# Kernel tuning notes

Measured on AMD Instinct MI355X. Metric: run time of the kernel, lower is better.

## Reference

```python
import jax, jax.numpy as jnp
import numpy as np

E, K, D, H, C = 32768, 32, 128, 4, 10
DH = D // H

def setup_inputs() -> dict:
    key = jax.random.key(0)
    ks = jax.random.split(key, 9)
    s = 1.0 / np.sqrt(D)
    return {
        "edge_feats": jax.random.normal(ks[0], (E, D), jnp.float32),
        "Wq": jax.random.normal(ks[1], (D, D), jnp.float32) * s,
        "Wk": jax.random.normal(ks[2], (D, D), jnp.float32) * s,
        "Wv": jax.random.normal(ks[3], (D, D), jnp.float32) * s,
        "Wo": jax.random.normal(ks[4], (D, D), jnp.float32) * s,
        "W1": jax.random.normal(ks[5], (D, D), jnp.float32) * s,
        "b1": jnp.zeros((D,), jnp.float32),
        "W2": jax.random.normal(ks[6], (D, C), jnp.float32) * s,
        "b2": jnp.zeros((C,), jnp.float32),
        "edge_adj": jax.random.randint(ks[7], (E, K), 0, E, jnp.int32),
    }

def reference(edge_feats, Wq, Wk, Wv, Wo, W1, b1, W2, b2, edge_adj):
    # Edge attention: each edge attends over its K adjacent edges.
    q = (edge_feats @ Wq).reshape(E, H, DH)                 # [E,H,dh]
    k_all = edge_feats @ Wk                                  # [E,D]
    v_all = edge_feats @ Wv                                  # [E,D]
    kn = k_all[edge_adj].reshape(E, K, H, DH)                # gather [E,K,H,dh]
    vn = v_all[edge_adj].reshape(E, K, H, DH)                # gather [E,K,H,dh]
    scores = jnp.einsum("ehd,ekhd->ehk", q, kn) / np.sqrt(DH)
    attn = jax.nn.softmax(scores, axis=-1)                   # [E,H,K]
    ctx = jnp.einsum("ehk,ekhd->ehd", attn, vn).reshape(E, D)
    edge_out = ctx @ Wo                                       # [E,D]
    # classifier: Linear -> GELU -> Linear
    h = jax.nn.gelu(edge_out @ W1 + b1)
    logits = h @ W2 + b2                                      # [E,C]
    return logits
```

## Files before the change

### kernel.cpp

```cpp
#include <hip/hip_runtime.h>
#include <hip/hip_bf16.h>

constexpr int E_EDGES = 32768;
constexpr int DIM = 128;

using bf16x8 = __attribute__((ext_vector_type(8))) short;
using f32x4  = __attribute__((ext_vector_type(4))) float;
using f32x2  = __attribute__((ext_vector_type(2))) float;
typedef unsigned int uint4v __attribute__((ext_vector_type(4)));
typedef unsigned int uint2v __attribute__((ext_vector_type(2)));

__device__ inline float bflo(unsigned u) { return __uint_as_float(u << 16); }
__device__ inline float bfhi(unsigned u) { return __uint_as_float(u & 0xffff0000u); }
__device__ inline f32x2 bf2f2(unsigned u) {
    f32x2 r;
    r[0] = __uint_as_float(u << 16);
    r[1] = __uint_as_float(u & 0xffff0000u);
    return r;
}
__device__ inline f32x2 fma2(f32x2 a, f32x2 b, f32x2 c) {
    return __builtin_elementwise_fma(a, b, c);
}
__device__ inline unsigned pk_bf2(float a, float b) {
    __hip_bfloat162 h = __float22bfloat162_rn(make_float2(a, b));
    return *(unsigned*)&h;
}

#if __has_builtin(__builtin_amdgcn_fdot2_f32_bf16)
typedef __bf16 bf16x2v __attribute__((ext_vector_type(2)));
__device__ inline float dot2bf(unsigned a, unsigned b, float c) {
    return __builtin_amdgcn_fdot2_f32_bf16(__builtin_bit_cast(bf16x2v, a),
                                           __builtin_bit_cast(bf16x2v, b),
                                           c, false);
}
#else
__device__ inline float dot2bf(unsigned a, unsigned b, float c) {
    float r = fmaf(bflo(a), bflo(b), c);
    return fmaf(bfhi(a), bfhi(b), r);
}
#endif

__global__ __launch_bounds__(256) void k_prep(
    const float* __restrict__ Wq, const float* __restrict__ Wk,
    const float* __restrict__ Wv, const float* __restrict__ Wo,
    const float* __restrict__ W1, __hip_bfloat16* __restrict__ Wt,
    __hip_bfloat16* __restrict__ wft) {
    const int b = blockIdx.x;
    const int t = threadIdx.x;
    if (b < 3) {
        const float* W = (b == 0) ? Wq : (b == 1) ? Wk : Wv;
        __hip_bfloat16* dst = Wt + b * 16384;
#pragma unroll
        for (int i = 0; i < 8; ++i) {
            int idx = i * 2048 + t * 8;
            int k = idx >> 7, n0 = idx & 127;
            float4 f0 = *(const float4*)(W + k * 128 + n0);
            float4 f1 = *(const float4*)(W + k * 128 + n0 + 4);
            float f[8] = {f0.x, f0.y, f0.z, f0.w, f1.x, f1.y, f1.z, f1.w};
#pragma unroll
            for (int j = 0; j < 8; ++j)
                dst[(n0 + j) * 128 + k] = __float2bfloat16(f[j]);
        }
    } else {
        int idx = (b - 3) * 256 + t;
        int r = idx >> 7, c = idx & 127;
        float acc = 0.f;
#pragma unroll 16
        for (int k = 0; k < 128; ++k)
            acc = fmaf(Wo[r * 128 + k], W1[k * 128 + c], acc);
        wft[c * 128 + r] = __float2bfloat16(acc);
    }
}

__global__ __launch_bounds__(256) void k_qkv(
    const float* __restrict__ feats, const __hip_bfloat16* __restrict__ Wt,
    __hip_bfloat16* __restrict__ qp, __hip_bfloat16* __restrict__ kp,
    __hip_bfloat16* __restrict__ vp) {
    __shared__ short Als[8192];
    __shared__ short Bls[16384];

    const int t = threadIdx.x;
    const int lane = t & 63;
    const int w = t >> 6;
    const int wm = w >> 1, wn = w & 1;
    const int row0 = blockIdx.x * 64;

#pragma unroll
    for (int i = 0; i < 4; ++i) {
        int idx = (i * 256 + t) * 8;
        int r = idx >> 7, k0 = idx & 127;
        float4 f0 = *(const float4*)(feats + (size_t)(row0 + r) * DIM + k0);
        float4 f1 = *(const float4*)(feats + (size_t)(row0 + r) * DIM + k0 + 4);
        uint4 o = make_uint4(pk_bf2(f0.x, f0.y), pk_bf2(f0.z, f0.w),
                             pk_bf2(f1.x, f1.y), pk_bf2(f1.z, f1.w));
        *(uint4*)&Als[(r * 128 + k0) ^ ((r & 7) << 3)] = o;
    }
#pragma unroll
    for (int i = 0; i < 8; ++i) {
        int idx = i * 2048 + t * 8;
        int n = idx >> 7, k0 = idx & 127;
        uint4 v = *(const uint4*)(Wt + n * 128 + k0);
        *(uint4*)&Bls[(n * 128 + k0) ^ ((n & 7) << 3)] = v;
    }
    __syncthreads();

    bf16x8 afr[2][4];
#pragma unroll
    for (int m = 0; m < 2; ++m)
#pragma unroll
        for (int ks = 0; ks < 4; ++ks) {
            int r = wm * 32 + m * 16 + (lane & 15);
            int kb = ks * 32 + (lane >> 4) * 8;
            afr[m][ks] = *(bf16x8*)&Als[(r * 128 + kb) ^ ((r & 7) << 3)];
        }

    for (int proj = 0; proj < 3; ++proj) {
        f32x4 acc[2][4];
#pragma unroll
        for (int m = 0; m < 2; ++m)
#pragma unroll
            for (int n = 0; n < 4; ++n) acc[m][n] = (f32x4){0.f, 0.f, 0.f, 0.f};

#pragma unroll
        for (int ks = 0; ks < 4; ++ks) {
            bf16x8 bfr[4];
#pragma unroll
            for (int n = 0; n < 4; ++n) {
                int nn = wn * 64 + n * 16 + (lane & 15);
                int kb = ks * 32 + (lane >> 4) * 8;
                bfr[n] = *(bf16x8*)&Bls[(nn * 128 + kb) ^ ((nn & 7) << 3)];
            }
#pragma unroll
            for (int m = 0; m < 2; ++m)
#pragma unroll
                for (int n = 0; n < 4; ++n)
                    acc[m][n] = __builtin_amdgcn_mfma_f32_16x16x32_bf16(
                        afr[m][ks], bfr[n], acc[m][n], 0, 0, 0);
        }

        __syncthreads();

#pragma unroll
        for (int m = 0; m < 2; ++m) {
#pragma unroll
            for (int n = 0; n < 4; ++n) {
                int c = wn * 64 + n * 16 + (lane & 15);
#pragma unroll
                for (int r = 0; r < 4; ++r) {
                    int lr = wm * 32 + m * 16 + (lane >> 4) * 4 + r;
                    Als[(lr * 128 + c) ^ ((lr & 7) << 3)] =
                        (short)__bfloat16_as_ushort(__float2bfloat16(acc[m][n][r]));
                }
            }
        }
        if (proj < 2) {
#pragma unroll
            for (int i = 0; i < 8; ++i) {
                int idx = i * 2048 + t * 8;
                int n = idx >> 7, k0 = idx & 127;
                uint4 v = *(const uint4*)(Wt + (proj + 1) * 16384 + n * 128 + k0);
                *(uint4*)&Bls[(n * 128 + k0) ^ ((n & 7) << 3)] = v;
            }
        }
        __syncthreads();

        {
            __hip_bfloat16* dst = (proj == 0) ? qp : (proj == 1) ? kp : vp;
#pragma unroll
            for (int i = 0; i < 4; ++i) {
                int id = i * 256 + t;
                int r = id >> 4;
                int c0 = (id & 15) * 8;
                uint4 v4 = *(uint4*)&Als[(r * 128 + c0) ^ ((r & 7) << 3)];
                int h = c0 >> 5, pr = h & 1;
                int slot = ((h >> 1) << 5) + (c0 & 31);
                *(uint4*)(dst + ((size_t)pr * E_EDGES + row0 + r) * 64 + slot) = v4;
            }
        }
    }
}

__global__ __launch_bounds__(256) void k_attn(
    const __hip_bfloat16* __restrict__ qp, const __hip_bfloat16* __restrict__ kp,
    const __hip_bfloat16* __restrict__ vp, const int* __restrict__ adj,
    __hip_bfloat16* __restrict__ ctxb) {
    const int pass = blockIdx.y;
    const int lane = threadIdx.x & 63;
    const int e = blockIdx.x * 4 + (threadIdx.x >> 6);
    const int n = lane & 31;
    const int g = lane >> 5;

    int adjv = 0;
    if (lane < 32) adjv = __builtin_nontemporal_load(adj + e * 32 + lane);

    const uint4v* qr =
        (const uint4v*)(qp + ((size_t)pass * E_EDGES + e) * 64 + g * 32);
    uint4v qu[4];
#pragma unroll
    for (int j = 0; j < 4; ++j) qu[j] = __builtin_nontemporal_load(qr + j);

    const int row = __shfl(adjv, n, 64);
    const uint4* kr =
        (const uint4*)(kp + ((size_t)pass * E_EDGES + row) * 64 + g * 32);
    float s0 = 0.f;
#pragma unroll
    for (int j = 0; j < 4; ++j) {
        uint4 u = kr[j];
        s0 = dot2bf(qu[j][0], u.x, s0);
        s0 = dot2bf(qu[j][1], u.y, s0);
        s0 = dot2bf(qu[j][2], u.z, s0);
        s0 = dot2bf(qu[j][3], u.w, s0);
    }
    s0 *= 0.17677669529663689f;

    float m0 = s0;
#pragma unroll
    for (int off = 16; off; off >>= 1) m0 = fmaxf(m0, __shfl_xor(m0, off));
    float e0 = __expf(s0 - m0);
    float sum0 = e0;
#pragma unroll
    for (int off = 16; off; off >>= 1) sum0 += __shfl_xor(sum0, off);
    const float wgt = e0 / sum0;

    const int rsel = lane >> 3;
    const int csel = lane & 7;
    const int gi = csel >> 2;
    f32x2 c01 = {0.f, 0.f}, c23 = {0.f, 0.f}, c45 = {0.f, 0.f}, c67 = {0.f, 0.f};
#pragma unroll
    for (int i = 0; i < 4; ++i) {
        int nn = i * 8 + rsel;
        float a = __shfl(wgt, gi * 32 + nn, 64);
        int r2 = __shfl(adjv, nn, 64);
        uint4 u = *(const uint4*)(vp + ((size_t)pass * E_EDGES + r2) * 64 + csel * 8);
        f32x2 a2 = {a, a};
        c01 = fma2(a2, bf2f2(u.x), c01);
        c23 = fma2(a2, bf2f2(u.y), c23);
        c45 = fma2(a2, bf2f2(u.z), c45);
        c67 = fma2(a2, bf2f2(u.w), c67);
    }
    float c[8] = {c01[0], c01[1], c23[0], c23[1], c45[0], c45[1], c67[0], c67[1]};
#pragma unroll
    for (int off = 8; off <= 32; off <<= 1)
#pragma unroll
        for (int j = 0; j < 8; ++j) c[j] += __shfl_xor(c[j], off);

    if (lane < 8) {
        int h2 = pass + 2 * (lane >> 2);
        uint4v o;
        o[0] = pk_bf2(c[0], c[1]);
        o[1] = pk_bf2(c[2], c[3]);
        o[2] = pk_bf2(c[4], c[5]);
        o[3] = pk_bf2(c[6], c[7]);
        __builtin_nontemporal_store(
            o, (uint4v*)(ctxb + (size_t)e * DIM + h2 * 32 + (lane & 3) * 8));
    }
}

__global__ __launch_bounds__(256) void k_mlp(
    const __hip_bfloat16* __restrict__ ctxb, const __hip_bfloat16* __restrict__ wft,
    const float* __restrict__ b1, const float* __restrict__ W2,
    const float* __restrict__ b2, float* __restrict__ out) {
    __shared__ short Als[8192];
    __shared__ short Bls[16384];
    __shared__ float w2s[1280];
    __shared__ float b1s[128];
    __shared__ float b2s[16];

    const int t = threadIdx.x;
    const int lane = t & 63;
    const int w = t >> 6;
    const int wm = w >> 1, wn = w & 1;
    const int row0 = blockIdx.x * 64;

#pragma unroll
    for (int i = 0; i < 4; ++i) {
        int idx = (i * 256 + t) * 8;
        int r = idx >> 7, k0 = idx & 127;
        uint4 v = *(const uint4*)(ctxb + (size_t)(row0 + r) * DIM + k0);
        *(uint4*)&Als[(r * 128 + k0) ^ ((r & 7) << 3)] = v;
    }
#pragma unroll
    for (int i = 0; i < 8; ++i) {
        int idx = i * 2048 + t * 8;
        int n = idx >> 7, k0 = idx & 127;
        uint4 v = *(const uint4*)(wft + n * 128 + k0);
        *(uint4*)&Bls[(n * 128 + k0) ^ ((n & 7) << 3)] = v;
    }
    for (int i = t; i < 1280; i += 256) w2s[i] = W2[i];
    if (t < 128) b1s[t] = b1[t];
    if (t < 10) b2s[t] = b2[t];
    __syncthreads();

    f32x4 acc[2][4];
#pragma unroll
    for (int m = 0; m < 2; ++m)
#pragma unroll
        for (int n = 0; n < 4; ++n) acc[m][n] = (f32x4){0.f, 0.f, 0.f, 0.f};

#pragma unroll
    for (int ks = 0; ks < 4; ++ks) {
        bf16x8 afr[2], bfr[4];
#pragma unroll
        for (int m = 0; m < 2; ++m) {
            int r = wm * 32 + m * 16 + (lane & 15);
            int kb = ks * 32 + (lane >> 4) * 8;
            afr[m] = *(bf16x8*)&Als[(r * 128 + kb) ^ ((r & 7) << 3)];
        }
#pragma unroll
        for (int n = 0; n < 4; ++n) {
            int nn = wn * 64 + n * 16 + (lane & 15);
            int kb = ks * 32 + (lane >> 4) * 8;
            bfr[n] = *(bf16x8*)&Bls[(nn * 128 + kb) ^ ((nn & 7) << 3)];
        }
#pragma unroll
        for (int m = 0; m < 2; ++m)
#pragma unroll
            for (int n = 0; n < 4; ++n)
                acc[m][n] = __builtin_amdgcn_mfma_f32_16x16x32_bf16(
                    afr[m], bfr[n], acc[m][n], 0, 0, 0);
    }

    __syncthreads();
#pragma unroll
    for (int m = 0; m < 2; ++m) {
        int lr0 = wm * 32 + m * 16 + (lane >> 4) * 4;
#pragma unroll
        for (int n = 0; n < 4; ++n) {
            int c = wn * 64 + n * 16 + (lane & 15);
            float bc = b1s[c];
#pragma unroll
            for (int r = 0; r < 4; ++r) {
                float x = acc[m][n][r] + bc;
                float u = 0.7978845608028654f * (x + 0.044715f * x * x * x);
                float ex = __expf(2.f * u);
                float th = 1.f - 2.f / (ex + 1.f);
                float h = 0.5f * x * (1.f + th);
                int lr = lr0 + r;
                Als[(lr * 128 + c) ^ ((lr & 7) << 3)] =
                    (short)(__bfloat16_as_ushort(__float2bfloat16(h)));
            }
        }
    }
    __syncthreads();

    for (int idx = t; idx < 640; idx += 256) {
        int r = idx / 10, c = idx - r * 10;
        float a = b2s[c];
#pragma unroll 8
        for (int kk = 0; kk < 128; ++kk) {
            float hv = __uint_as_float(
                ((unsigned)(unsigned short)Als[(r * 128 + kk) ^ ((r & 7) << 3)]) << 16);
            a = fmaf(hv, w2s[kk * 10 + c], a);
        }
        out[(size_t)(row0 + r) * 10 + c] = a;
    }
}

extern "C" void kernel_launch(void* const* d_in, const int* in_sizes, int n_in,
                              void* d_out, int out_size, void* d_ws, size_t ws_size,
                              hipStream_t stream) {
    const float* feats = (const float*)d_in[0];
    const float* Wq    = (const float*)d_in[1];
    const float* Wk    = (const float*)d_in[2];
    const float* Wv    = (const float*)d_in[3];
    const float* Wo    = (const float*)d_in[4];
    const float* W1    = (const float*)d_in[5];
    const float* b1    = (const float*)d_in[6];
    const float* W2    = (const float*)d_in[7];
    const float* b2    = (const float*)d_in[8];
    const int*   adj   = (const int*)d_in[9];
    float* out = (float*)d_out;

    const size_t ED2 = (size_t)E_EDGES * 64;
    __hip_bfloat16* base = (__hip_bfloat16*)d_ws;
    __hip_bfloat16* qp   = base;
    __hip_bfloat16* kp   = qp + 2 * ED2;
    __hip_bfloat16* vp   = kp + 2 * ED2;
    __hip_bfloat16* ctxb = vp + 2 * ED2;
    __hip_bfloat16* wt   = ctxb + 2 * ED2;
    __hip_bfloat16* wft  = wt + 3 * 16384;

    k_prep<<<67, 256, 0, stream>>>(Wq, Wk, Wv, Wo, W1, wt, wft);
    k_qkv<<<E_EDGES / 64, 256, 0, stream>>>(feats, wt, qp, kp, vp);
    k_attn<<<dim3(E_EDGES / 4, 2), 256, 0, stream>>>(qp, kp, vp, adj, ctxb);
    k_mlp<<<E_EDGES / 64, 256, 0, stream>>>(ctxb, wft, b1, W2, b2, out);
}
```

Before: 97.00 us.

## Read GEMM weight fragments directly from global memory instead of LDS staging

In the QKV and MLP kernels, the B-operand weight tiles are no longer staged through shared memory. Each wave now loads its bf16x8 fragments straight from global or L2, which removes the 32 KB LDS buffer and the barriers around it and should allow more blocks per CU. The QKV kernel also writes its outputs directly from the accumulators as scattered 2-byte stores instead of staging them through LDS for coalesced 16-byte stores. The trade-off is more global or L2 traffic for weights shared by every block, and narrower, less coalesced output writes.

Result: slower. 105.8 us (+9.1%).

```diff
diff --git a/kernel.cpp b/kernel.cpp
--- a/kernel.cpp
+++ b/kernel.cpp
@@ -77,7 +77,6 @@
     __hip_bfloat16* __restrict__ qp, __hip_bfloat16* __restrict__ kp,
     __hip_bfloat16* __restrict__ vp) {
     __shared__ short Als[8192];
-    __shared__ short Bls[16384];
 
     const int t = threadIdx.x;
     const int lane = t & 63;
@@ -95,13 +94,6 @@
                              pk_bf2(f1.x, f1.y), pk_bf2(f1.z, f1.w));
         *(uint4*)&Als[(r * 128 + k0) ^ ((r & 7) << 3)] = o;
     }
-#pragma unroll
-    for (int i = 0; i < 8; ++i) {
-        int idx = i * 2048 + t * 8;
-        int n = idx >> 7, k0 = idx & 127;
-        uint4 v = *(const uint4*)(Wt + n * 128 + k0);
-        *(uint4*)&Bls[(n * 128 + k0) ^ ((n & 7) << 3)] = v;
-    }
     __syncthreads();
 
     bf16x8 afr[2][4];
@@ -128,7 +120,7 @@
             for (int n = 0; n < 4; ++n) {
                 int nn = wn * 64 + n * 16 + (lane & 15);
                 int kb = ks * 32 + (lane >> 4) * 8;
-                bfr[n] = *(bf16x8*)&Bls[(nn * 128 + kb) ^ ((nn & 7) << 3)];
+                bfr[n] = *(const bf16x8*)(Wt + proj * 16384 + nn * 128 + kb);
             }
 #pragma unroll
             for (int m = 0; m < 2; ++m)
@@ -138,43 +130,22 @@
                         afr[m][ks], bfr[n], acc[m][n], 0, 0, 0);
         }
 
-        __syncthreads();
-
-#pragma unroll
-        for (int m = 0; m < 2; ++m) {
+        {
+            __hip_bfloat16* dst = (proj == 0) ? qp : (proj == 1) ? kp : vp;
 #pragma unroll
             for (int n = 0; n < 4; ++n) {
                 int c = wn * 64 + n * 16 + (lane & 15);
-#pragma unroll
-                for (int r = 0; r < 4; ++r) {
-                    int lr = wm * 32 + m * 16 + (lane >> 4) * 4 + r;
-                    Als[(lr * 128 + c) ^ ((lr & 7) << 3)] =
-                        (short)__bfloat16_as_ushort(__float2bfloat16(acc[m][n][r]));
+                int h = c >> 5, pr = h & 1;
+                int slot = ((h >> 1) << 5) + (c & 31);
+                size_t base = (size_t)pr * E_EDGES * 64 + slot;
+#pragma unroll
+                for (int m = 0; m < 2; ++m) {
+                    int rb = row0 + wm * 32 + m * 16 + (lane >> 4) * 4;
+#pragma unroll
+                    for (int r = 0; r < 4; ++r)
+                        dst[base + (size_t)(rb + r) * 64] =
+                            __float2bfloat16(acc[m][n][r]);
                 }
-            }
-        }
-        if (proj < 2) {
-#pragma unroll
-            for (int i = 0; i < 8; ++i) {
-                int idx = i * 2048 + t * 8;
-                int n = idx >> 7, k0 = idx & 127;
-                uint4 v = *(const uint4*)(Wt + (proj + 1) * 16384 + n * 128 + k0);
-                *(uint4*)&Bls[(n * 128 + k0) ^ ((n & 7) << 3)] = v;
-            }
-        }
-        __syncthreads();
-
-        {
-            __hip_bfloat16* dst = (proj == 0) ? qp : (proj == 1) ? kp : vp;
-#pragma unroll
-            for (int i = 0; i < 4; ++i) {
-                int id = i * 256 + t;
-                int r = id >> 4;
-                int c0 = (id & 15) * 8;
-                uint4 v4 = *(uint4*)&Als[(r * 128 + c0) ^ ((r & 7) << 3)];
-                int h = c0 >> 5, pr = h & 1;
-                int slot = ((h >> 1) << 5) + (c0 & 31);
-                *(uint4*)(dst + ((size_t)pr * E_EDGES + row0 + r) * 64 + slot) = v4;
             }
         }
     }
@@ -261,7 +232,6 @@
     const float* __restrict__ b1, const float* __restrict__ W2,
     const float* __restrict__ b2, float* __restrict__ out) {
     __shared__ short Als[8192];
-    __shared__ short Bls[16384];
     __shared__ float w2s[1280];
     __shared__ float b1s[128];
     __shared__ float b2s[16];
@@ -279,45 +249,42 @@
         uint4 v = *(const uint4*)(ctxb + (size_t)(row0 + r) * DIM + k0);
         *(uint4*)&Als[(r * 128 + k0) ^ ((r & 7) << 3)] = v;
     }
-#pragma unroll
-    for (int i = 0; i < 8; ++i) {
-        int idx = i * 2048 + t * 8;
-        int n = idx >> 7, k0 = idx & 127;
-        uint4 v = *(const uint4*)(wft + n * 128 + k0);
-        *(uint4*)&Bls[(n * 128 + k0) ^ ((n & 7) << 3)] = v;
-    }
     for (int i = t; i < 1280; i += 256) w2s[i] = W2[i];
     if (t < 128) b1s[t] = b1[t];
     if (t < 10) b2s[t] = b2[t];
     __syncthreads();
 
-    f32x4 acc[2][4];
+    bf16x8 afr[2][4];
 #pragma unroll
     for (int m = 0; m < 2; ++m)
 #pragma unroll
-        for (int n = 0; n < 4; ++n) acc[m][n] = (f32x4){0.f, 0.f, 0.f, 0.f};
-
-#pragma unroll
-    for (int ks = 0; ks < 4; ++ks) {
-        bf16x8 afr[2], bfr[4];
-#pragma unroll
-        for (int m = 0; m < 2; ++m) {
+        for (int ks = 0; ks < 4; ++ks) {
             int r = wm * 32 + m * 16 + (lane & 15);
             int kb = ks * 32 + (lane >> 4) * 8;
-            afr[m] = *(bf16x8*)&Als[(r * 128 + kb) ^ ((r & 7) << 3)];
-        }
+            afr[m][ks] = *(bf16x8*)&Als[(r * 128 + kb) ^ ((r & 7) << 3)];
+        }
+
+    f32x4 acc[2][4];
+#pragma unroll
+    for (int m = 0; m < 2; ++m)
+#pragma unroll
+        for (int n = 0; n < 4; ++n) acc[m][n] = (f32x4){0.f, 0.f, 0.f, 0.f};
+
+#pragma unroll
+    for (int ks = 0; ks < 4; ++ks) {
+        bf16x8 bfr[4];
 #pragma unroll
         for (int n = 0; n < 4; ++n) {
             int nn = wn * 64 + n * 16 + (lane & 15);
             int kb = ks * 32 + (lane >> 4) * 8;
-            bfr[n] = *(bf16x8*)&Bls[(nn * 128 + kb) ^ ((nn & 7) << 3)];
+            bfr[n] = *(const bf16x8*)(wft + nn * 128 + kb);
         }
 #pragma unroll
         for (int m = 0; m < 2; ++m)
 #pragma unroll
             for (int n = 0; n < 4; ++n)
                 acc[m][n] = __builtin_amdgcn_mfma_f32_16x16x32_bf16(
-                    afr[m], bfr[n], acc[m][n], 0, 0, 0);
+                    afr[m][ks], bfr[n], acc[m][n], 0, 0, 0);
     }
 
     __syncthreads();
```
